# Kernel optimization log

Measured on AMD Instinct MI355X. Metric: run time of the kernel, lower is better.

Reference implementation:

```python
import jax, jax.numpy as jnp
import numpy as np

N_IMG = 512
N_ANGLES = 180


def _bilinear(img, sy, sx):
    """Bilinear sample img at float coords (sy, sx); zero outside the image."""
    n = img.shape[0]
    y0 = jnp.floor(sy)
    x0 = jnp.floor(sx)
    wy = sy - y0
    wx = sx - x0
    y0i = y0.astype(jnp.int32)
    x0i = x0.astype(jnp.int32)

    def gather(yi, xi):
        valid = (yi >= 0) & (yi < n) & (xi >= 0) & (xi < n)
        yc = jnp.clip(yi, 0, n - 1)
        xc = jnp.clip(xi, 0, n - 1)
        return jnp.where(valid, img[yc, xc], jnp.zeros((), img.dtype))

    v00 = gather(y0i, x0i)
    v01 = gather(y0i, x0i + 1)
    v10 = gather(y0i + 1, x0i)
    v11 = gather(y0i + 1, x0i + 1)
    return (v00 * (1 - wy) * (1 - wx) + v01 * (1 - wy) * wx
            + v10 * wy * (1 - wx) + v11 * wy * wx)


def _radon(img, angles):
    """skimage-style radon: rotate image by each angle, sum along axis 0.
    Returns sinogram of shape (n_detectors, n_angles) = (N, len(angles))."""
    n = img.shape[0]
    c = (n - 1) * 0.5  # rotation about image center
    coords = jnp.arange(n, dtype=img.dtype) - c
    yc, xc = jnp.meshgrid(coords, coords, indexing="ij")  # (N, N)

    def one_angle(theta_deg):
        t = jnp.deg2rad(theta_deg.astype(img.dtype))
        co, si = jnp.cos(t), jnp.sin(t)
        # inverse-rotation sampling coordinates (CCW rotation of the image)
        sx = co * xc + si * yc + c
        sy = -si * xc + co * yc + c
        rotated = _bilinear(img, sy, sx)  # (N, N)
        return rotated.sum(axis=0)        # projection along detector rows -> (N,)

    sino = jax.vmap(one_angle)(angles)  # (n_angles, N)
    return sino.T                        # (N, n_angles)


def setup_inputs() -> dict:
    key = jax.random.key(0)
    img = jax.random.uniform(key, (N_IMG, N_IMG), dtype=jnp.float32)  # nonnegative PET activity
    angles = jnp.arange(N_ANGLES, dtype=jnp.int32)  # degrees 0..179 (skimage default)
    return {"img": img, "angles": angles}


def reference(img, angles):
    return _radon(img, angles)
```

## Files before the change

kernel.cpp:

```cpp
#include <hip/hip_runtime.h>
#include <hip/hip_fp16.h>
#include <stdint.h>

#define N 512
#define NA 180
#define PP 708
#define PR 704
#define POFF 96

#define WS_IMGVP  0
#define WS_IMGVPT (PR * PP)
#define WS_TAB    (2 * PR * PP)
#define WS_FLAGS  (WS_TAB + 4 * NA)

typedef _Float16 hh2 __attribute__((ext_vector_type(2)));
union H2U { uint32_t u; hh2 h; };

__device__ __forceinline__ hh2 cvt_pkrtz(float a, float b) {
    return __builtin_bit_cast(hh2, __builtin_amdgcn_cvt_pkrtz(a, b));
}

__global__ __launch_bounds__(256) void pad_kernel(const float* __restrict__ img,
                                                  const int* __restrict__ angles,
                                                  uint32_t* __restrict__ imgVP,
                                                  uint32_t* __restrict__ imgVPT,
                                                  float4* __restrict__ tab,
                                                  int* __restrict__ flags) {
    __shared__ float lds[33 * 34];
    const int tid = threadIdx.x;
    const int bx = blockIdx.x, by = blockIdx.y;

    if (bx == 0 && by == 0 && tid < NA) {
        float t = (float)angles[tid] * 0.017453292519943295f;
        float si = sinf(t), co = cosf(t);
        int useT = fabsf(si) > fabsf(co);
        float4 e;
        if (useT) { e.x = co; e.y = -si; e.z = si; e.w = co; }
        else      { e.x = si; e.y = co;  e.z = co; e.w = -si; }
        tab[tid] = e;
        flags[tid] = useT;
    }

    for (int idx = tid; idx < 33 * 33; idx += 256) {
        int r = idx / 33, cc = idx - r * 33;
        int y = by * 32 + r - POFF, x = bx * 32 + cc - POFF;
        bool in = ((unsigned)y < N) && ((unsigned)x < N);
        lds[r * 34 + cc] = in ? img[y * N + x] : 0.0f;
    }
    __syncthreads();
    const int r0 = tid >> 5, cl = tid & 31;
#pragma unroll
    for (int j = 0; j < 4; ++j) {
        int row = j * 8 + r0;
        float v0 = lds[row * 34 + cl], v1 = lds[(row + 1) * 34 + cl];
        __half2 h = __halves2half2(__float2half(v0), __float2half(v1));
        imgVP[(size_t)(by * 32 + row) * PP + bx * 32 + cl] = *(uint32_t*)&h;
        float t0 = lds[cl * 34 + row], t1 = lds[cl * 34 + row + 1];
        __half2 ht = __halves2half2(__float2half(t0), __float2half(t1));
        imgVPT[(size_t)(bx * 32 + row) * PP + by * 32 + cl] = *(uint32_t*)&ht;
    }
}

__global__ __launch_bounds__(256) void radon_kernel(const uint32_t* __restrict__ imgVP,
                                                    const uint32_t* __restrict__ imgVPT,
                                                    const float4* __restrict__ tab,
                                                    const int* __restrict__ flags,
                                                    float* __restrict__ out) {
    __shared__ float red[256];

    const int tid = threadIdx.x;
    const int dl  = tid & 63;
    const int q   = tid >> 6;
    const int d0  = blockIdx.x * 64;
    const int a   = blockIdx.y;

    const float c = 255.5f;
    const float4 tb = tab[a];
    const float au = tb.x, bus = tb.y, av = tb.z, bvs = tb.w;
    const uint32_t* __restrict__ src = flags[a] ? imgVPT : imgVP;

    const float xcl = (float)(d0 + dl) - c;
    const float buP = fmaf(bus, xcl, c + (float)POFF) - au * c;
    const float bvP = fmaf(bvs, xcl, c + (float)POFF) - av * c;

    int iLo = q * 128, iHi = q * 128 + 127;
    if (fabsf(au) > 1e-6f) {
        float ia = 1.0f / au;
        float t0 = (94.0f - buP) * ia, t1 = (609.0f - buP) * ia;
        float lo = fminf(t0, t1), hi = fmaxf(t0, t1);
        iLo = max(iLo, (int)ceilf(lo));
        iHi = min(iHi, (int)floorf(hi));
    } else if (buP < 94.0f || buP > 609.0f) {
        iHi = iLo - 1;
    }
    if (fabsf(av) > 1e-6f) {
        float ia = 1.0f / av;
        float t0 = (94.0f - bvP) * ia, t1 = (609.0f - bvP) * ia;
        float lo = fminf(t0, t1), hi = fmaxf(t0, t1);
        iLo = max(iLo, (int)ceilf(lo));
        iHi = min(iHi, (int)floorf(hi));
    } else if (bvP < 94.0f || bvP > 609.0f) {
        iHi = iLo - 1;
    }

    float s = 0.0f;
    float fi = (float)iLo;
    auto sample = [&]() {
        float u = fmaf(au, fi, buP);
        float v = fmaf(av, fi, bvP);
        float wx = __builtin_amdgcn_fractf(u);
        float wy = __builtin_amdgcn_fractf(v);
        int iu = (int)u, iv = (int)v;
        const uint32_t* p = src + iv * PP + iu;
        H2U P0, P1;
        P0.u = p[0];
        P1.u = p[1];
        hh2 wyv = cvt_pkrtz(1.0f - wy, wy);
        float mx0 = __builtin_amdgcn_fdot2(wyv, P0.h, 0.0f, false);
        float mx1 = __builtin_amdgcn_fdot2(wyv, P1.h, 0.0f, false);
        s = fmaf(wx, mx1 - mx0, s + mx0);
        fi += 1.0f;
    };

    if (iHi >= iLo) {
        const int cnt = iHi - iLo + 1;
        const int n4  = cnt >> 2;
        for (int it = 0; it < n4; ++it) {
#pragma unroll
            for (int k = 0; k < 4; ++k) sample();
        }
        const int rem = cnt & 3;
        for (int r2 = 0; r2 < rem; ++r2) sample();
    }

    red[tid] = s;
    __syncthreads();
    if (tid < 64) {
        float r = red[tid] + red[tid + 64] + red[tid + 128] + red[tid + 192];
        out[(d0 + tid) * NA + a] = r;
    }
}

extern "C" void kernel_launch(void* const* d_in, const int* in_sizes, int n_in,
                              void* d_out, int out_size, void* d_ws, size_t ws_size,
                              hipStream_t stream) {
    const float* img  = (const float*)d_in[0];
    const int* angles = (const int*)d_in[1];
    float* out = (float*)d_out;
    float* ws  = (float*)d_ws;

    uint32_t* imgVP  = (uint32_t*)(ws + WS_IMGVP);
    uint32_t* imgVPT = (uint32_t*)(ws + WS_IMGVPT);
    float4*   tab    = (float4*)(ws + WS_TAB);
    int*      flags  = (int*)(ws + WS_FLAGS);

    dim3 pgrid(22, 22);
    pad_kernel<<<pgrid, 256, 0, stream>>>(img, angles, imgVP, imgVPT, tab, flags);

    dim3 grid(N / 64, NA);
    radon_kernel<<<grid, 256, 0, stream>>>(imgVP, imgVPT, tab, flags, out);
}
```

Before: 101.5 us.

## Pack 2x2 bilinear neighborhoods into uint2 and interleave samples across lanes

```diff
diff --git a/kernel.cpp b/kernel.cpp
--- a/kernel.cpp
+++ b/kernel.cpp
@@ -8,9 +8,9 @@
 #define PR 704
 #define POFF 96
 
-#define WS_IMGVP  0
-#define WS_IMGVPT (PR * PP)
-#define WS_TAB    (2 * PR * PP)
+#define WS_IMGQ   0
+#define WS_IMGQT  (PR * PP * 2)
+#define WS_TAB    (2 * PR * PP * 2)
 #define WS_FLAGS  (WS_TAB + 4 * NA)
 
 typedef _Float16 hh2 __attribute__((ext_vector_type(2)));
@@ -20,10 +20,15 @@
     return __builtin_bit_cast(hh2, __builtin_amdgcn_cvt_pkrtz(a, b));
 }
 
+__device__ __forceinline__ uint32_t packh2(float a, float b) {
+    __half2 h = __halves2half2(__float2half(a), __float2half(b));
+    return *(uint32_t*)&h;
+}
+
 __global__ __launch_bounds__(256) void pad_kernel(const float* __restrict__ img,
                                                   const int* __restrict__ angles,
-                                                  uint32_t* __restrict__ imgVP,
-                                                  uint32_t* __restrict__ imgVPT,
+                                                  uint2* __restrict__ imgQ,
+                                                  uint2* __restrict__ imgQT,
                                                   float4* __restrict__ tab,
                                                   int* __restrict__ flags) {
     __shared__ float lds[33 * 34];
@@ -52,38 +57,40 @@
 #pragma unroll
     for (int j = 0; j < 4; ++j) {
         int row = j * 8 + r0;
-        float v0 = lds[row * 34 + cl], v1 = lds[(row + 1) * 34 + cl];
-        __half2 h = __halves2half2(__float2half(v0), __float2half(v1));
-        imgVP[(size_t)(by * 32 + row) * PP + bx * 32 + cl] = *(uint32_t*)&h;
-        float t0 = lds[cl * 34 + row], t1 = lds[cl * 34 + row + 1];
-        __half2 ht = __halves2half2(__float2half(t0), __float2half(t1));
-        imgVPT[(size_t)(bx * 32 + row) * PP + by * 32 + cl] = *(uint32_t*)&ht;
+        uint2 qv;
+        qv.x = packh2(lds[row * 34 + cl],     lds[(row + 1) * 34 + cl]);
+        qv.y = packh2(lds[row * 34 + cl + 1], lds[(row + 1) * 34 + cl + 1]);
+        imgQ[(size_t)(by * 32 + row) * PP + bx * 32 + cl] = qv;
+        uint2 qt;
+        qt.x = packh2(lds[cl * 34 + row],       lds[cl * 34 + row + 1]);
+        qt.y = packh2(lds[(cl + 1) * 34 + row], lds[(cl + 1) * 34 + row + 1]);
+        imgQT[(size_t)(bx * 32 + row) * PP + by * 32 + cl] = qt;
     }
 }
 
-__global__ __launch_bounds__(256) void radon_kernel(const uint32_t* __restrict__ imgVP,
-                                                    const uint32_t* __restrict__ imgVPT,
+__global__ __launch_bounds__(256) void radon_kernel(const uint2* __restrict__ imgQ,
+                                                    const uint2* __restrict__ imgQT,
                                                     const float4* __restrict__ tab,
                                                     const int* __restrict__ flags,
                                                     float* __restrict__ out) {
-    __shared__ float red[256];
-
-    const int tid = threadIdx.x;
-    const int dl  = tid & 63;
-    const int q   = tid >> 6;
-    const int d0  = blockIdx.x * 64;
-    const int a   = blockIdx.y;
+    const int tid  = threadIdx.x;
+    const int lane = tid & 63;
+    const int wave = tid >> 6;
+    const int dd   = lane >> 3;
+    const int ii   = lane & 7;
+    const int a    = blockIdx.y;
+    const int d    = blockIdx.x * 32 + wave * 8 + dd;
 
     const float c = 255.5f;
     const float4 tb = tab[a];
     const float au = tb.x, bus = tb.y, av = tb.z, bvs = tb.w;
-    const uint32_t* __restrict__ src = flags[a] ? imgVPT : imgVP;
+    const uint2* __restrict__ src = flags[a] ? imgQT : imgQ;
 
-    const float xcl = (float)(d0 + dl) - c;
+    const float xcl = (float)d - c;
     const float buP = fmaf(bus, xcl, c + (float)POFF) - au * c;
     const float bvP = fmaf(bvs, xcl, c + (float)POFF) - av * c;
 
-    int iLo = q * 128, iHi = q * 128 + 127;
+    int iLo = 0, iHi = N - 1;
     if (fabsf(au) > 1e-6f) {
         float ia = 1.0f / au;
         float t0 = (94.0f - buP) * ia, t1 = (609.0f - buP) * ia;
@@ -104,41 +111,27 @@
     }
 
     float s = 0.0f;
-    float fi = (float)iLo;
-    auto sample = [&]() {
+    float fi = (float)(iLo + ii);
+    for (int i = iLo + ii; i <= iHi; i += 8) {
         float u = fmaf(au, fi, buP);
         float v = fmaf(av, fi, bvP);
         float wx = __builtin_amdgcn_fractf(u);
         float wy = __builtin_amdgcn_fractf(v);
         int iu = (int)u, iv = (int)v;
-        const uint32_t* p = src + iv * PP + iu;
-        H2U P0, P1;
-        P0.u = p[0];
-        P1.u = p[1];
+        uint2 q = src[iv * PP + iu];
+        H2U Pl, Pr;
+        Pl.u = q.x; Pr.u = q.y;
         hh2 wyv = cvt_pkrtz(1.0f - wy, wy);
-        float mx0 = __builtin_amdgcn_fdot2(wyv, P0.h, 0.0f, false);
-        float mx1 = __builtin_amdgcn_fdot2(wyv, P1.h, 0.0f, false);
+        float mx0 = __builtin_amdgcn_fdot2(wyv, Pl.h, 0.0f, false);
+        float mx1 = __builtin_amdgcn_fdot2(wyv, Pr.h, 0.0f, false);
         s = fmaf(wx, mx1 - mx0, s + mx0);
-        fi += 1.0f;
-    };
-
-    if (iHi >= iLo) {
-        const int cnt = iHi - iLo + 1;
-        const int n4  = cnt >> 2;
-        for (int it = 0; it < n4; ++it) {
-#pragma unroll
-            for (int k = 0; k < 4; ++k) sample();
-        }
-        const int rem = cnt & 3;
-        for (int r2 = 0; r2 < rem; ++r2) sample();
+        fi += 8.0f;
     }
 
-    red[tid] = s;
-    __syncthreads();
-    if (tid < 64) {
-        float r = red[tid] + red[tid + 64] + red[tid + 128] + red[tid + 192];
-        out[(d0 + tid) * NA + a] = r;
-    }
+    s += __shfl_xor(s, 1);
+    s += __shfl_xor(s, 2);
+    s += __shfl_xor(s, 4);
+    if (ii == 0) out[d * NA + a] = s;
 }
 
 extern "C" void kernel_launch(void* const* d_in, const int* in_sizes, int n_in,
@@ -149,14 +142,14 @@
     float* out = (float*)d_out;
     float* ws  = (float*)d_ws;
 
-    uint32_t* imgVP  = (uint32_t*)(ws + WS_IMGVP);
-    uint32_t* imgVPT = (uint32_t*)(ws + WS_IMGVPT);
-    float4*   tab    = (float4*)(ws + WS_TAB);
-    int*      flags  = (int*)(ws + WS_FLAGS);
+    uint2*  imgQ  = (uint2*)(ws + WS_IMGQ);
+    uint2*  imgQT = (uint2*)(ws + WS_IMGQT);
+    float4* tab   = (float4*)(ws + WS_TAB);
+    int*    flags = (int*)(ws + WS_FLAGS);
 
     dim3 pgrid(22, 22);
-    pad_kernel<<<pgrid, 256, 0, stream>>>(img, angles, imgVP, imgVPT, tab, flags);
+    pad_kernel<<<pgrid, 256, 0, stream>>>(img, angles, imgQ, imgQT, tab, flags);
 
-    dim3 grid(N / 64, NA);
-    radon_kernel<<<grid, 256, 0, stream>>>(imgVP, imgVPT, tab, flags, out);
+    dim3 grid(N / 32, NA);
+    radon_kernel<<<grid, 256, 0, stream>>>(imgQ, imgQT, tab, flags, out);
 }
```

Result: slower. 119.8 us (+18.1%).
